# Performance work log

Hardware: AMD Instinct MI355X
Metric: run time of the kernel (lower is better)

The kernel has to match this reference:

```python
import jax, jax.numpy as jnp
import numpy as np

IN_DIM = 128
LAYER_DIMS = [128, 128]
NUM_SAMPLES = [25, 10]
L0 = 3072
NEG_WEIGHT = 1.0


def setup_inputs() -> dict:
    key = jax.random.key(0)
    ks = jax.random.split(key, 12)
    feat = jax.random.normal(ks[0], (L0, IN_DIM), dtype=jnp.float32)
    nodes = jax.random.randint(ks[1], (L0,), 0, L0)
    nb0 = jnp.arange(L0)
    nb1 = jax.random.randint(ks[2], (L0 * 10,), 0, L0)
    nb2 = jax.random.randint(ks[3], (L0 * 10 * 25,), 0, L0)
    src_idx = jax.random.randint(ks[4], (1024,), 0, L0)
    pos_idx = jax.random.randint(ks[5], (1024,), 0, L0)
    neg_idx = jax.random.randint(ks[6], (512,), 0, L0)
    g = 0.05
    # mean aggregator weights: layer0 in=IN_DIM, layer1 in=2*128 (concat)
    w_self_0 = jax.random.normal(ks[7], (IN_DIM, 128), jnp.float32) * g
    w_neigh_0 = jax.random.normal(ks[8], (IN_DIM, 128), jnp.float32) * g
    w_self_1 = jax.random.normal(ks[9], (256, 128), jnp.float32) * g
    w_neigh_1 = jax.random.normal(ks[10], (256, 128), jnp.float32) * g
    return dict(nodes=nodes, feat=feat, src_idx=src_idx, pos_idx=pos_idx,
                neg_idx=neg_idx, nb0=nb0, nb1=nb1, nb2=nb2,
                w_self_0=w_self_0, w_neigh_0=w_neigh_0,
                w_self_1=w_self_1, w_neigh_1=w_neigh_1)


def _aggregate(hidden, params):
    # GraphSAGE layer stack: at layer l, combine each hop with the mean of its
    # sampled neighbors, concat self/neigh transforms, relu except last layer.
    num_layers = len(NUM_SAMPLES)
    for layer in range(num_layers):
        w_self, w_neigh = params[layer]
        is_last = layer == num_layers - 1
        next_hidden = []
        for hop in range(num_layers - layer):
            s = NUM_SAMPLES[num_layers - hop - 1]
            self_v = hidden[hop]  # [n, d]
            neigh = hidden[hop + 1].reshape(self_v.shape[0], s, self_v.shape[1])
            neigh_mean = jnp.mean(neigh, axis=1)
            h = jnp.concatenate([self_v @ w_self, neigh_mean @ w_neigh], axis=1)
            if not is_last:
                h = jax.nn.relu(h)
            next_hidden.append(h)
        hidden = next_hidden
    return hidden[0]


def _l2_normalize(x, eps=1e-12):
    return x * jax.lax.rsqrt(jnp.maximum(jnp.sum(x * x, axis=1, keepdims=True), eps))


def reference(nodes, feat, src_idx, pos_idx, neg_idx, nb0, nb1, nb2,
              w_self_0, w_neigh_0, w_self_1, w_neigh_1):
    hidden = [feat[nb0], feat[nb1], feat[nb2]]
    params = [(w_self_0, w_neigh_0), (w_self_1, w_neigh_1)]
    output = _aggregate(hidden, params)          # [L0, 256]
    output = _l2_normalize(output)
    src_emb = output[src_idx]                    # [B, 256]
    pos_emb = output[pos_idx]
    neg_emb = output[neg_idx]                    # [Nneg, 256]

    aff = jnp.sum(src_emb * pos_emb, axis=1)     # [B]
    neg_aff = src_emb @ neg_emb.T                # [B, Nneg]

    # MRR via double argsort (tf double top_k equivalent; ties -> positive last)
    aff_all = jnp.concatenate([neg_aff, aff[:, None]], axis=1)
    order = jnp.argsort(-aff_all, axis=1, stable=True)
    ranks = jnp.argsort(order, axis=1, stable=True)
    mrr = jnp.mean(1.0 / (ranks[:, -1].astype(jnp.float32) + 1.0))

    # sigmoid cross-entropy: labels 1 -> softplus(-x); labels 0 -> softplus(x)
    true_xent = jax.nn.softplus(-aff)
    neg_xent = jax.nn.softplus(neg_aff)
    loss = jnp.sum(true_xent) + NEG_WEIGHT * jnp.sum(neg_xent)
    loss = loss / jnp.asarray(src_emb.shape[0], jnp.float32)
    return src_emb, loss, mrr
```

## Files before the change

### kernel.cpp

```cpp
#include <hip/hip_runtime.h>
#include <math.h>

#define L0      3072
#define BATCH   1024
#define NNEG    512


__device__ __forceinline__ float bf2f(unsigned short u) {
  return __uint_as_float(((unsigned)u) << 16);
}
__device__ __forceinline__ void store_out(float v, float* p) { *p = v; }
__device__ __forceinline__ void store_out(float v, unsigned short* p) {
  unsigned x = __float_as_uint(v);
  *p = (unsigned short)((x + 0x7fff + ((x >> 16) & 1)) >> 16);
}

template<int K, int AW, int HOFF, bool NORM, typename OutT>
__global__ __launch_bounds__(512) void k_mm(
    const float* __restrict__ Ain,
    const float* __restrict__ W0, const float* __restrict__ W1,
    OutT* __restrict__ Out, const int ldo, const int outHalfOff) {
  __shared__ float AT[6 * AW];
  __shared__ float rs[8][3];
  const int t = threadIdx.x;
  const int base = blockIdx.x * 6;
  {
    const float4* __restrict__ src = (const float4*)(Ain + base * AW);
    float4* __restrict__ dst = (float4*)AT;
    for (int idx = t; idx < 6 * AW / 4; idx += 512) dst[idx] = src[idx];
  }
  __syncthreads();

  const int wave = t >> 6;
  const int half = wave >> 2;
  const int colg = (wave >> 1) & 1;
  const int rowg = wave & 1;
  const int rg = rowg * 3;
  const int col = colg * 64 + (t & 63);
  const float* __restrict__ W = (half ? W1 : W0) + col;
  const float* __restrict__ A0 = AT + rg * AW + half * HOFF;

  float acc[3] = {0.f, 0.f, 0.f};
#pragma unroll 4
  for (int d = 0; d < K; d += 4) {
    float4 a[3];
#pragma unroll
    for (int r = 0; r < 3; ++r) a[r] = *(const float4*)&A0[r * AW + d];
    float w[4];
#pragma unroll
    for (int i2 = 0; i2 < 4; ++i2) w[i2] = W[(d + i2) * 128];
#pragma unroll
    for (int i2 = 0; i2 < 4; ++i2)
#pragma unroll
      for (int r = 0; r < 3; ++r)
        acc[r] = fmaf(((const float*)&a[r])[i2], w[i2], acc[r]);
  }

  float scale[3] = {1.f, 1.f, 1.f};
  if (NORM) {
    float p[3];
#pragma unroll
    for (int r = 0; r < 3; ++r) p[r] = acc[r] * acc[r];
#pragma unroll
    for (int off = 32; off > 0; off >>= 1)
#pragma unroll
      for (int r = 0; r < 3; ++r) p[r] += __shfl_xor(p[r], off, 64);
    if ((t & 63) == 0) { rs[wave][0] = p[0]; rs[wave][1] = p[1]; rs[wave][2] = p[2]; }
    __syncthreads();
#pragma unroll
    for (int r = 0; r < 3; ++r) {
      const float s = rs[rowg][r] + rs[rowg + 2][r] + rs[rowg + 4][r] + rs[rowg + 6][r];
      scale[r] = rsqrtf(fmaxf(s, 1e-12f));
    }
  }
  OutT* __restrict__ O = Out + half * outHalfOff;
#pragma unroll
  for (int r = 0; r < 3; ++r)
    store_out(acc[r] * scale[r], &O[(base + rg + r) * ldo + col]);
}

__global__ __launch_bounds__(640) void k_aggregate(
    const unsigned short* __restrict__ X0, const unsigned short* __restrict__ Y0,
    const int* __restrict__ nb0, const int* __restrict__ nb1,
    const int* __restrict__ nb2, float* __restrict__ H) {
  __shared__ float gB[10][128], gC[10][128], gD[10][128];
  const int i = blockIdx.x;
  const int t = threadIdx.x;
  const int n0 = nb0[i];
  const int j = t >> 6;
  const int lam = t & 63;
  const int r = i * 10 + j;
  int myidx = 0;
  if (lam < 25) myidx = nb2[r * 25 + lam];
  else if (lam == 25) myidx = nb1[r];
  const int c8 = lam & 15;
  const int sub = lam >> 4;

  float d8[8];
#pragma unroll
  for (int e = 0; e < 8; ++e) d8[e] = 0.f;
#pragma unroll
  for (int m = 0; m < 7; ++m) {
    const int k = sub + 4 * m;
    const int ridx = __shfl(myidx, k, 64);
    if (k < 25) {
      const float4 raw = *(const float4*)(Y0 + ridx * 128 + c8 * 8);
      const unsigned short* u = (const unsigned short*)&raw;
#pragma unroll
      for (int e = 0; e < 8; ++e) d8[e] += bf2f(u[e]);
    }
  }
#pragma unroll
  for (int e = 0; e < 8; ++e) d8[e] += __shfl_xor(d8[e], 16, 64);
#pragma unroll
  for (int e = 0; e < 8; ++e) d8[e] += __shfl_xor(d8[e], 32, 64);

  const int r1 = __shfl(myidx, 25, 64);
  if (sub == 0) {
#pragma unroll
    for (int e = 0; e < 8; ++e) gD[j][c8 * 8 + e] = fmaxf(d8[e] * 0.04f, 0.f);
    const float4 raw = *(const float4*)(Y0 + r1 * 128 + c8 * 8);
    const unsigned short* u = (const unsigned short*)&raw;
#pragma unroll
    for (int e = 0; e < 8; ++e) gB[j][c8 * 8 + e] = bf2f(u[e]);
  } else if (sub == 1) {
    const float4 raw = *(const float4*)(X0 + r1 * 128 + c8 * 8);
    const unsigned short* u = (const unsigned short*)&raw;
#pragma unroll
    for (int e = 0; e < 8; ++e) gC[j][c8 * 8 + e] = fmaxf(bf2f(u[e]), 0.f);
  }
  __syncthreads();

  if (t < 512) {
    const int q = t >> 7, c = t & 127;
    float v;
    if (q == 0) {
      v = fmaxf(bf2f(X0[n0 * 128 + c]), 0.f);
    } else {
      const float* g = (q == 1) ? &gB[0][0] : (q == 2) ? &gC[0][0] : &gD[0][0];
      float s = 0.f;
#pragma unroll
      for (int jj = 0; jj < 10; ++jj) s += g[jj * 128 + c];
      v = s * 0.1f;
      if (q == 1) v = fmaxf(v, 0.f);
    }
    H[i * 512 + t] = v;
  }
}

__device__ __forceinline__ float softplusf(float x) {
  return fmaxf(x, 0.f) + log1pf(expf(-fabsf(x)));
}

__global__ __launch_bounds__(512) void k_neg(
    const float* __restrict__ O,
    const int* __restrict__ src_idx, const int* __restrict__ pos_idx,
    const int* __restrict__ neg_idx,
    float* __restrict__ out_src, int* __restrict__ rankPart,
    float* __restrict__ spPosPart, float* __restrict__ spNegPart) {
  __shared__ float SP[64 * 260];
  __shared__ float BT[256 * 64];
  __shared__ float affL[32];
  __shared__ int cntL[32];
  __shared__ float wsum[16];
  const int t = threadIdx.x;
  const int bid = blockIdx.x;
  const int rowBase = (bid >> 3) * 32;
  const int colBase = (bid & 7) * 64;
  const bool first = ((bid & 7) == 0);

  {
    const float4* __restrict__ s4 = (const float4*)O;
#pragma unroll
    for (int idx = t; idx < 64 * 64; idx += 512) {
      const int row = idx >> 6, c4 = idx & 63;
      const int rid = (row < 32) ? src_idx[rowBase + row]
                                 : pos_idx[rowBase + row - 32];
      *(float4*)&SP[row * 260 + c4 * 4] = s4[rid * 64 + c4];
    }
  }
  {
    const float4* __restrict__ s4 = (const float4*)O;
#pragma unroll
    for (int idx = t; idx < 64 * 64; idx += 512) {
      const int j = idx & 63, c4 = idx >> 6;
      const float4 v = s4[neg_idx[colBase + j] * 64 + c4];
      BT[(4 * c4 + 0) * 64 + j] = v.x;
      BT[(4 * c4 + 1) * 64 + j] = v.y;
      BT[(4 * c4 + 2) * 64 + j] = v.z;
      BT[(4 * c4 + 3) * 64 + j] = v.w;
    }
  }
  if (first) {
    const float4* __restrict__ s4 = (const float4*)O;
    float4* __restrict__ d4o = (float4*)out_src;
#pragma unroll
    for (int idx = t; idx < 32 * 64; idx += 512) {
      const int rr = idx >> 6, c4 = idx & 63;
      d4o[(rowBase + rr) * 64 + c4] = s4[src_idx[rowBase + rr] * 64 + c4];
    }
  }
  __syncthreads();

  const int tc = t & 31;
  const int rowg = t >> 5;
  const float* __restrict__ A0 = SP + rowg * 260;
  const float* __restrict__ A1 = SP + (rowg + 16) * 260;
  const float* __restrict__ SV = SP + t * 260;
  const float* __restrict__ PV = SP + (32 + t) * 260;

  float acc00 = 0.f, acc01 = 0.f, acc10 = 0.f, acc11 = 0.f, aff = 0.f;
#pragma unroll 4
  for (int d4 = 0; d4 < 64; ++d4) {
    const int dd = d4 * 4;
    const float4 a0 = *(const float4*)&A0[dd];
    const float4 a1 = *(const float4*)&A1[dd];
    float2 b[4];
#pragma unroll
    for (int i2 = 0; i2 < 4; ++i2)
      b[i2] = *(const float2*)&BT[(dd + i2) * 64 + 2 * tc];
    float4 sv, pv;
    if (t < 32) {
      sv = *(const float4*)&SV[dd];
      pv = *(const float4*)&PV[dd];
    }
#pragma unroll
    for (int i2 = 0; i2 < 4; ++i2) {
      const float va0 = ((const float*)&a0)[i2];
      const float va1 = ((const float*)&a1)[i2];
      acc00 = fmaf(va0, b[i2].x, acc00);
      acc01 = fmaf(va0, b[i2].y, acc01);
      acc10 = fmaf(va1, b[i2].x, acc10);
      acc11 = fmaf(va1, b[i2].y, acc11);
      if (t < 32)
        aff = fmaf(((const float*)&sv)[i2], ((const float*)&pv)[i2], aff);
    }
  }
  if (t < 32) affL[t] = aff;
  __syncthreads();

  float sp = softplusf(acc00) + softplusf(acc01) +
             softplusf(acc10) + softplusf(acc11);
  const float av0 = affL[rowg], av1 = affL[rowg + 16];
  int c0 = ((acc00 >= av0) ? 1 : 0) + ((acc01 >= av0) ? 1 : 0);
  int c1 = ((acc10 >= av1) ? 1 : 0) + ((acc11 >= av1) ? 1 : 0);
#pragma unroll
  for (int off = 16; off > 0; off >>= 1) {
    sp += __shfl_down(sp, off, 32);
    c0 += __shfl_down(c0, off, 32);
    c1 += __shfl_down(c1, off, 32);
  }
  if ((t & 31) == 0) {
    cntL[rowg] = c0;
    cntL[rowg + 16] = c1;
    wsum[rowg] = sp;
  }
  __syncthreads();

  if (t < 32) rankPart[(bid & 7) * 1024 + rowBase + t] = cntL[t];
  if (t == 0) {
    float sn = 0.f;
#pragma unroll
    for (int w = 0; w < 16; ++w) sn += wsum[w];
    spNegPart[bid] = sn;
  }
  if (first && t == 0) {
    float ps = 0.f;
#pragma unroll
    for (int r = 0; r < 32; ++r) ps += softplusf(-affL[r]);
    spPosPart[bid >> 3] = ps;
  }
}

__global__ __launch_bounds__(256) void k_finalize(
    const int* __restrict__ rankPart, const float* __restrict__ spPosPart,
    const float* __restrict__ spNegPart, float* __restrict__ out) {
  __shared__ float wa[4], wb[4];
  const int t = threadIdx.x;
  float s = 0.f;
  for (int i = t; i < BATCH; i += 256) {
    int rv = 0;
#pragma unroll
    for (int p = 0; p < 8; ++p) rv += rankPart[p * 1024 + i];
    s += 1.f / (float)(rv + 1);
  }
  float l = 0.f;
  if (t < 256) l += spNegPart[t];
  if (t < 32) l += spPosPart[t];
#pragma unroll
  for (int off = 32; off > 0; off >>= 1) {
    s += __shfl_down(s, off, 64);
    l += __shfl_down(l, off, 64);
  }
  if ((t & 63) == 0) { wa[t >> 6] = s; wb[t >> 6] = l; }
  __syncthreads();
  if (t == 0) {
    out[BATCH * 256]     = (wb[0] + wb[1] + wb[2] + wb[3]) * (1.f / 1024.f);
    out[BATCH * 256 + 1] = (wa[0] + wa[1] + wa[2] + wa[3]) * (1.f / 1024.f);
  }
}

extern "C" void kernel_launch(void* const* d_in, const int* in_sizes, int n_in,
                              void* d_out, int out_size, void* d_ws, size_t ws_size,
                              hipStream_t stream) {
  const float* feat   = (const float*)d_in[1];
  const int* src_idx  = (const int*)d_in[2];
  const int* pos_idx  = (const int*)d_in[3];
  const int* neg_idx  = (const int*)d_in[4];
  const int* nb0      = (const int*)d_in[5];
  const int* nb1      = (const int*)d_in[6];
  const int* nb2      = (const int*)d_in[7];
  const float* ws0    = (const float*)d_in[8];
  const float* wn0    = (const float*)d_in[9];
  const float* ws1    = (const float*)d_in[10];
  const float* wn1    = (const float*)d_in[11];

  float* wsf = (float*)d_ws;
  unsigned short* X0 = (unsigned short*)d_ws;
  unsigned short* Y0 = X0 + 393216;
  float* H       = wsf + 393216;
  float* R       = wsf + 1966080;
  float* spPosP  = wsf + 2752512;
  float* spNegP  = wsf + 2752640;
  int*   rankP   = (int*)(wsf + 2753664);
  float* out     = (float*)d_out;

  k_mm<128, 128, 0, false, unsigned short><<<L0 / 6, 512, 0, stream>>>(
      feat, ws0, wn0, X0, 128, 393216);
  k_aggregate<<<L0, 640, 0, stream>>>(X0, Y0, nb0, nb1, nb2, H);
  k_mm<256, 512, 256, true, float><<<L0 / 6, 512, 0, stream>>>(
      H, ws1, wn1, R, 256, 128);
  k_neg<<<256, 512, 0, stream>>>(
      R, src_idx, pos_idx, neg_idx, out, rankP, spPosP, spNegP);
  k_finalize<<<1, 256, 0, stream>>>(rankP, spPosP, spNegP, out);
}
```

Measured before the change: 157.7 us.

## Fuse neighbor aggregation with layer-1 matmul and L2 normalization

Merges the aggregation kernel and the second-layer matmul into a single kernel. Each block gathers neighbor means for 4 output nodes into shared memory, builds the 512-wide hidden rows there, then multiplies by the layer-1 weights and normalizes each row in place. This removes the H intermediate round-trip through global memory and one kernel launch. The cost is fewer rows per block (4 instead of 6) and 2 accumulators per thread, so weight reuse drops. About 70KB of shared memory per block may also limit occupancy.

```diff
diff --git a/kernel.cpp b/kernel.cpp
--- a/kernel.cpp
+++ b/kernel.cpp
@@ -79,72 +79,120 @@
     store_out(acc[r] * scale[r], &O[(base + rg + r) * ldo + col]);
 }
 
-__global__ __launch_bounds__(640) void k_aggregate(
+__global__ __launch_bounds__(512) void k_aggmm(
     const unsigned short* __restrict__ X0, const unsigned short* __restrict__ Y0,
     const int* __restrict__ nb0, const int* __restrict__ nb1,
-    const int* __restrict__ nb2, float* __restrict__ H) {
-  __shared__ float gB[10][128], gC[10][128], gD[10][128];
-  const int i = blockIdx.x;
+    const int* __restrict__ nb2,
+    const float* __restrict__ ws1, const float* __restrict__ wn1,
+    float* __restrict__ R) {
+  __shared__ float gB[40][128], gC[40][128], gD[40][128];
+  __shared__ float HT[4 * 512];
+  __shared__ float rs[8][2];
   const int t = threadIdx.x;
-  const int n0 = nb0[i];
-  const int j = t >> 6;
-  const int lam = t & 63;
-  const int r = i * 10 + j;
-  int myidx = 0;
-  if (lam < 25) myidx = nb2[r * 25 + lam];
-  else if (lam == 25) myidx = nb1[r];
-  const int c8 = lam & 15;
-  const int sub = lam >> 4;
-
-  float d8[8];
-#pragma unroll
-  for (int e = 0; e < 8; ++e) d8[e] = 0.f;
-#pragma unroll
-  for (int m = 0; m < 7; ++m) {
-    const int k = sub + 4 * m;
-    const int ridx = __shfl(myidx, k, 64);
-    if (k < 25) {
-      const float4 raw = *(const float4*)(Y0 + ridx * 128 + c8 * 8);
+  const int wave = t >> 6, lam = t & 63;
+  const int base = blockIdx.x * 4;
+  const int c8 = lam & 15, sub = lam >> 4;
+
+#pragma unroll
+  for (int k = 0; k < 5; ++k) {
+    const int tau = wave + k * 8;
+    const int li = tau / 10, j = tau - li * 10;
+    const int r = (base + li) * 10 + j;
+    int myidx = 0;
+    if (lam < 25) myidx = nb2[r * 25 + lam];
+    else if (lam == 25) myidx = nb1[r];
+
+    float d8[8];
+#pragma unroll
+    for (int e = 0; e < 8; ++e) d8[e] = 0.f;
+#pragma unroll
+    for (int m = 0; m < 7; ++m) {
+      const int kk = sub + 4 * m;
+      const int ridx = __shfl(myidx, kk, 64);
+      if (kk < 25) {
+        const float4 raw = *(const float4*)(Y0 + ridx * 128 + c8 * 8);
+        const unsigned short* u = (const unsigned short*)&raw;
+#pragma unroll
+        for (int e = 0; e < 8; ++e) d8[e] += bf2f(u[e]);
+      }
+    }
+#pragma unroll
+    for (int e = 0; e < 8; ++e) d8[e] += __shfl_xor(d8[e], 16, 64);
+#pragma unroll
+    for (int e = 0; e < 8; ++e) d8[e] += __shfl_xor(d8[e], 32, 64);
+
+    const int r1 = __shfl(myidx, 25, 64);
+    if (sub == 0) {
+#pragma unroll
+      for (int e = 0; e < 8; ++e) gD[tau][c8 * 8 + e] = fmaxf(d8[e] * 0.04f, 0.f);
+      const float4 raw = *(const float4*)(Y0 + r1 * 128 + c8 * 8);
       const unsigned short* u = (const unsigned short*)&raw;
 #pragma unroll
-      for (int e = 0; e < 8; ++e) d8[e] += bf2f(u[e]);
-    }
-  }
-#pragma unroll
-  for (int e = 0; e < 8; ++e) d8[e] += __shfl_xor(d8[e], 16, 64);
-#pragma unroll
-  for (int e = 0; e < 8; ++e) d8[e] += __shfl_xor(d8[e], 32, 64);
-
-  const int r1 = __shfl(myidx, 25, 64);
-  if (sub == 0) {
-#pragma unroll
-    for (int e = 0; e < 8; ++e) gD[j][c8 * 8 + e] = fmaxf(d8[e] * 0.04f, 0.f);
-    const float4 raw = *(const float4*)(Y0 + r1 * 128 + c8 * 8);
-    const unsigned short* u = (const unsigned short*)&raw;
-#pragma unroll
-    for (int e = 0; e < 8; ++e) gB[j][c8 * 8 + e] = bf2f(u[e]);
-  } else if (sub == 1) {
-    const float4 raw = *(const float4*)(X0 + r1 * 128 + c8 * 8);
-    const unsigned short* u = (const unsigned short*)&raw;
-#pragma unroll
-    for (int e = 0; e < 8; ++e) gC[j][c8 * 8 + e] = fmaxf(bf2f(u[e]), 0.f);
-  }
-  __syncthreads();
-
-  if (t < 512) {
-    const int q = t >> 7, c = t & 127;
-    float v;
-    if (q == 0) {
-      v = fmaxf(bf2f(X0[n0 * 128 + c]), 0.f);
-    } else {
-      const float* g = (q == 1) ? &gB[0][0] : (q == 2) ? &gC[0][0] : &gD[0][0];
-      float s = 0.f;
-#pragma unroll
-      for (int jj = 0; jj < 10; ++jj) s += g[jj * 128 + c];
-      v = s * 0.1f;
-      if (q == 1) v = fmaxf(v, 0.f);
-    }
-    H[i * 512 + t] = v;
+      for (int e = 0; e < 8; ++e) gB[tau][c8 * 8 + e] = bf2f(u[e]);
+    } else if (sub == 1) {
+      const float4 raw = *(const float4*)(X0 + r1 * 128 + c8 * 8);
+      const unsigned short* u = (const unsigned short*)&raw;
+#pragma unroll
+      for (int e = 0; e < 8; ++e) gC[tau][c8 * 8 + e] = fmaxf(bf2f(u[e]), 0.f);
+    }
+  }
+  __syncthreads();
+
+  {
+    const int li = t >> 7, c = t & 127;
+    const int n0 = nb0[base + li];
+    float sB = 0.f, sC = 0.f, sD = 0.f;
+#pragma unroll
+    for (int jj = 0; jj < 10; ++jj) {
+      sB += gB[li * 10 + jj][c];
+      sC += gC[li * 10 + jj][c];
+      sD += gD[li * 10 + jj][c];
+    }
+    HT[li * 512 + c]       = fmaxf(bf2f(X0[n0 * 128 + c]), 0.f);
+    HT[li * 512 + 128 + c] = fmaxf(sB * 0.1f, 0.f);
+    HT[li * 512 + 256 + c] = sC * 0.1f;
+    HT[li * 512 + 384 + c] = sD * 0.1f;
+  }
+  __syncthreads();
+
+  const int half = wave >> 2;
+  const int colg = (wave >> 1) & 1;
+  const int rowg = wave & 1;
+  const int rg = rowg * 2;
+  const int col = colg * 64 + lam;
+  const float* __restrict__ W = (half ? wn1 : ws1) + col;
+  const float* __restrict__ A0 = HT + rg * 512 + half * 256;
+
+  float acc[2] = {0.f, 0.f};
+#pragma unroll 4
+  for (int d = 0; d < 256; d += 4) {
+    float4 a[2];
+#pragma unroll
+    for (int r = 0; r < 2; ++r) a[r] = *(const float4*)&A0[r * 512 + d];
+    float w[4];
+#pragma unroll
+    for (int i2 = 0; i2 < 4; ++i2) w[i2] = W[(d + i2) * 128];
+#pragma unroll
+    for (int i2 = 0; i2 < 4; ++i2)
+#pragma unroll
+      for (int r = 0; r < 2; ++r)
+        acc[r] = fmaf(((const float*)&a[r])[i2], w[i2], acc[r]);
+  }
+
+  float p[2];
+#pragma unroll
+  for (int r = 0; r < 2; ++r) p[r] = acc[r] * acc[r];
+#pragma unroll
+  for (int off = 32; off > 0; off >>= 1)
+#pragma unroll
+    for (int r = 0; r < 2; ++r) p[r] += __shfl_xor(p[r], off, 64);
+  if (lam == 0) { rs[wave][0] = p[0]; rs[wave][1] = p[1]; }
+  __syncthreads();
+#pragma unroll
+  for (int r = 0; r < 2; ++r) {
+    const float s = rs[rowg][r] + rs[rowg + 2][r] + rs[rowg + 4][r] + rs[rowg + 6][r];
+    const float scale = rsqrtf(fmaxf(s, 1e-12f));
+    R[(base + rg + r) * 256 + half * 128 + col] = acc[r] * scale;
   }
 }
 
@@ -318,7 +366,6 @@
   float* wsf = (float*)d_ws;
   unsigned short* X0 = (unsigned short*)d_ws;
   unsigned short* Y0 = X0 + 393216;
-  float* H       = wsf + 393216;
   float* R       = wsf + 1966080;
   float* spPosP  = wsf + 2752512;
   float* spNegP  = wsf + 2752640;
@@ -327,9 +374,8 @@
 
   k_mm<128, 128, 0, false, unsigned short><<<L0 / 6, 512, 0, stream>>>(
       feat, ws0, wn0, X0, 128, 393216);
-  k_aggregate<<<L0, 640, 0, stream>>>(X0, Y0, nb0, nb1, nb2, H);
-  k_mm<256, 512, 256, true, float><<<L0 / 6, 512, 0, stream>>>(
-      H, ws1, wn1, R, 256, 128);
+  k_aggmm<<<L0 / 4, 512, 0, stream>>>(
+      X0, Y0, nb0, nb1, nb2, ws1, wn1, R);
   k_neg<<<256, 512, 0, stream>>>(
       R, src_idx, pos_idx, neg_idx, out, rankP, spPosP, spNegP);
   k_finalize<<<1, 256, 0, stream>>>(rankP, spPosP, spNegP, out);
```

Result: no change. 155.9 us (-1.1%).
